# Performance work log

Hardware: AMD Instinct MI355X
Metric: run time of the kernel (lower is better)

## Reference

```python
import math
import jax, jax.numpy as jnp
import numpy as np

N, D, K = 8192, 256, 32


def setup_inputs() -> dict:
    key = jax.random.key(0)
    kx, kw, kb = jax.random.split(key, 3)
    x = jax.random.normal(kx, (N, D), dtype=jnp.float32)
    # params per _init_weights: w ~ N(1, 0.01), b ~ N(0, 0.01)
    w = 1.0 + 0.01 * jax.random.normal(kw, (K, D), dtype=jnp.float32)
    b = 0.01 * jax.random.normal(kb, (K, D), dtype=jnp.float32)
    return {"x": x, "w": w, "b": b}


def reference(x, w, b):
    # x: (N, D); w, b: (K, D)
    y1 = w[None, :, :] * (x[:, None, :] + b[None, :, :])        # (N, K, D)
    y2 = y1 * y1                                                 # (N, K, D)
    y4 = -0.5 * jnp.sum(y2, axis=-1)                             # (N, K)
    gamma = jax.nn.softmax(y4, axis=-1)                          # (N, K)
    y6 = (y2 - 1.0) * (1.0 / math.sqrt(2.0))                     # (N, K, D)
    g = gamma[:, :, None]                                        # (N, K, 1)
    n, kk, d = y1.shape
    sigma_part = (g * y6).reshape(n, kk * d)                     # (N, K*D)
    mu_part = (g * y1).reshape(n, kk * d)                        # (N, K*D)
    phi_patches = jnp.concatenate([sigma_part, mu_part], axis=-1)
    return jnp.mean(phi_patches, axis=0)                         # (2*K*D,)
```

## Files before the change

kernel.cpp:

```cpp
#include <hip/hip_runtime.h>
#include <math.h>

#define Nn 8192
#define Dd 256
#define Kk 32

#define P_OFF   0
#define P2_OFF  4194304
#define SP_OFF  4325376

__global__ __launch_bounds__(1024) void fused_kernel(const float* __restrict__ x,
                                                     const float* __restrict__ w,
                                                     const float* __restrict__ b,
                                                     float* __restrict__ ws) {
    __shared__ __align__(16) float4 uS4[64 * 33];
    __shared__ __align__(16) float4 vS4[64 * 33];
    __shared__ __align__(16) float4 xS4[32 * 64];
    __shared__ float  gS[1024];

    float* P  = ws + P_OFF;
    float* Sp = ws + SP_OFF;
    int tid = threadIdx.x;
    int blk = blockIdx.x;

    {
        const float* xg = x + (size_t)blk * 32 * Dd;
        #pragma unroll
        for (int i = 0; i < 2; ++i) {
            int e4 = tid + i * 1024;
            __builtin_amdgcn_global_load_lds(
                (const __attribute__((address_space(1))) void*)(xg + (size_t)e4 * 4),
                (__attribute__((address_space(3))) void*)(&xS4[e4]),
                16, 0, 0);
        }
    }

    {
        const float4* w4 = (const float4*)w;
        const float4* b4 = (const float4*)b;
        #pragma unroll
        for (int i = 0; i < 2; ++i) {
            int e4 = tid + i * 1024;
            int k  = e4 >> 6;
            int d4 = e4 & 63;
            float4 wv = w4[e4];
            float4 bv = b4[e4];
            float4 vv = {wv.x * bv.x, wv.y * bv.y, wv.z * bv.z, wv.w * bv.w};
            uS4[d4 * 33 + k] = wv;
            vS4[d4 * 33 + k] = vv;
        }
    }
    __syncthreads();

    {
        int lane = tid & 63;
        int wave = tid >> 6;
        int k = lane & 31;
        int h = lane >> 5;
        int r0 = wave * 2;

        const float4* xr0 = &xS4[(r0 + 0) * 64];
        const float4* xr1 = &xS4[(r0 + 1) * 64];

        float4 a0 = {0.f, 0.f, 0.f, 0.f}, a1 = a0;

        #pragma unroll 8
        for (int i = 0; i < 32; ++i) {
            int ii = h * 32 + i;
            float4 u  = uS4[ii * 33 + k];
            float4 v  = vS4[ii * 33 + k];
            float4 x0 = xr0[ii];
            float4 x1 = xr1[ii];
            float y;
            y = fmaf(u.x, x0.x, v.x); a0.x = fmaf(y, y, a0.x);
            y = fmaf(u.y, x0.y, v.y); a0.y = fmaf(y, y, a0.y);
            y = fmaf(u.z, x0.z, v.z); a0.z = fmaf(y, y, a0.z);
            y = fmaf(u.w, x0.w, v.w); a0.w = fmaf(y, y, a0.w);
            y = fmaf(u.x, x1.x, v.x); a1.x = fmaf(y, y, a1.x);
            y = fmaf(u.y, x1.y, v.y); a1.y = fmaf(y, y, a1.y);
            y = fmaf(u.z, x1.z, v.z); a1.z = fmaf(y, y, a1.z);
            y = fmaf(u.w, x1.w, v.w); a1.w = fmaf(y, y, a1.w);
        }

        float s0 = (a0.x + a0.y) + (a0.z + a0.w);
        float s1 = (a1.x + a1.y) + (a1.z + a1.w);
        s0 += __shfl_xor(s0, 32);
        s1 += __shfl_xor(s1, 32);
        float y40 = -0.5f * s0, y41 = -0.5f * s1;

        float m0 = y40, m1 = y41;
        #pragma unroll
        for (int o = 16; o >= 1; o >>= 1) {
            m0 = fmaxf(m0, __shfl_xor(m0, o));
            m1 = fmaxf(m1, __shfl_xor(m1, o));
        }
        float e0 = __expf(y40 - m0), e1 = __expf(y41 - m1);
        float t0 = e0, t1 = e1;
        #pragma unroll
        for (int o = 16; o >= 1; o >>= 1) {
            t0 += __shfl_xor(t0, o);
            t1 += __shfl_xor(t1, o);
        }
        if (h == 0) {
            gS[(r0 + 0) * 32 + k] = e0 / t0;
            gS[(r0 + 1) * 32 + k] = e1 / t1;
        }
    }
    __syncthreads();

    if (tid < 32) {
        float s0 = 0.f, s1 = 0.f, s2 = 0.f, s3 = 0.f;
        #pragma unroll
        for (int r = 0; r < 32; r += 4) {
            s0 += gS[(r + 0) * 32 + tid];
            s1 += gS[(r + 1) * 32 + tid];
            s2 += gS[(r + 2) * 32 + tid];
            s3 += gS[(r + 3) * 32 + tid];
        }
        Sp[tid * 256 + blk] = (s0 + s1) + (s2 + s3);
    }

    {
        int kq = tid >> 8;
        int d  = tid & 255;
        const float* xl = (const float*)xS4;
        const float4* gS4 = (const float4*)gS;

        float aG[8], aH[8];
        #pragma unroll
        for (int j = 0; j < 8; ++j) { aG[j] = 0.f; aH[j] = 0.f; }

        #pragma unroll 4
        for (int r = 0; r < 32; ++r) {
            float xv = xl[r * 256 + d];
            float xx = xv * xv;
            #pragma unroll
            for (int q = 0; q < 2; ++q) {
                float4 gv = gS4[r * 8 + kq * 2 + q];
                aG[4*q+0] = fmaf(gv.x, xv, aG[4*q+0]); aH[4*q+0] = fmaf(gv.x, xx, aH[4*q+0]);
                aG[4*q+1] = fmaf(gv.y, xv, aG[4*q+1]); aH[4*q+1] = fmaf(gv.y, xx, aH[4*q+1]);
                aG[4*q+2] = fmaf(gv.z, xv, aG[4*q+2]); aH[4*q+2] = fmaf(gv.z, xx, aH[4*q+2]);
                aG[4*q+3] = fmaf(gv.w, xv, aG[4*q+3]); aH[4*q+3] = fmaf(gv.w, xx, aH[4*q+3]);
            }
        }

        #pragma unroll
        for (int j = 0; j < 8; ++j) {
            int k = kq * 8 + j;
            P[((size_t)(k * 2 + 0) * 256 + blk) * 256 + d] = aG[j];
            P[((size_t)(k * 2 + 1) * 256 + blk) * 256 + d] = aH[j];
        }
    }
}

__global__ __launch_bounds__(256) void red1_kernel(float* __restrict__ ws) {
    const float* P = ws + P_OFF;
    float* P2 = ws + P2_OFF;
    int tid = threadIdx.x;
    int k  = blockIdx.x >> 4;
    int gh = (blockIdx.x >> 3) & 1;
    int c  = blockIdx.x & 7;

    const float* p = P + ((size_t)(k * 2 + gh) * 256 + c * 32) * 256 + tid;
    float s0 = 0.f, s1 = 0.f, s2 = 0.f, s3 = 0.f;
    #pragma unroll
    for (int i = 0; i < 32; i += 4) {
        s0 += p[(size_t)(i + 0) * 256];
        s1 += p[(size_t)(i + 1) * 256];
        s2 += p[(size_t)(i + 2) * 256];
        s3 += p[(size_t)(i + 3) * 256];
    }
    P2[((size_t)(k * 2 + gh) * 8 + c) * 256 + tid] = (s0 + s1) + (s2 + s3);
}

__global__ __launch_bounds__(256) void red2_kernel(const float* __restrict__ w,
                                                   const float* __restrict__ b,
                                                   const float* __restrict__ ws,
                                                   float* __restrict__ out) {
    const float* P2 = ws + P2_OFF;
    const float* Sp = ws + SP_OFF;
    __shared__ float sred[4];
    int k = blockIdx.x, d = threadIdx.x;

    float sv_part = Sp[k * 256 + d];
    #pragma unroll
    for (int o = 32; o >= 1; o >>= 1) sv_part += __shfl_xor(sv_part, o);
    if ((d & 63) == 0) sred[d >> 6] = sv_part;
    __syncthreads();
    float sv = (sred[0] + sred[1]) + (sred[2] + sred[3]);

    const float* pg = P2 + (size_t)(k * 2 + 0) * 8 * 256 + d;
    const float* ph = P2 + (size_t)(k * 2 + 1) * 8 * 256 + d;
    float Gv = 0.f, Hv = 0.f;
    #pragma unroll
    for (int c = 0; c < 8; ++c) {
        Gv += pg[c * 256];
        Hv += ph[c * 256];
    }

    int idx = k * Dd + d;
    float wv = w[idx], bv = b[idx];
    const float invN = 1.0f / 8192.0f;
    const float c2 = 0.70710678118654752440f * invN;
    float mu = wv * (Gv + bv * sv) * invN;
    float w2 = wv * wv;
    float sg = (w2 * (Hv + 2.0f * bv * Gv + bv * bv * sv) - sv) * c2;
    out[idx] = sg;
    out[Kk * Dd + idx] = mu;
}

extern "C" void kernel_launch(void* const* d_in, const int* in_sizes, int n_in,
                              void* d_out, int out_size, void* d_ws, size_t ws_size,
                              hipStream_t stream) {
    const float* x = (const float*)d_in[0];
    const float* w = (const float*)d_in[1];
    const float* b = (const float*)d_in[2];
    float* out = (float*)d_out;
    float* ws = (float*)d_ws;

    hipLaunchKernelGGL(fused_kernel, dim3(256), dim3(1024), 0, stream, x, w, b, ws);
    hipLaunchKernelGGL(red1_kernel,  dim3(512), dim3(256),  0, stream, ws);
    hipLaunchKernelGGL(red2_kernel,  dim3(32),  dim3(256),  0, stream, w, b, ws, out);
}
```

Before: 82.85 us.

## Reorganize distance phase: 4 rows per thread, XOR-swizzled w/b LDS, async w load

Each thread in the squared-distance phase now computes 4 rows × 1 component over a quarter of D, rather than 2 rows over half of D. This reuses each loaded u/v pair across more rows and cuts LDS traffic per FMA. The w/b tiles move from a padded transposed layout to a row-major layout with an XOR swizzle to avoid bank conflicts, and w is copied straight to LDS with global_load_lds. The change adds an extra LDS buffer and a __syncthreads, because partial sums go through shared memory before the softmax.

```diff
diff --git a/kernel.cpp b/kernel.cpp
--- a/kernel.cpp
+++ b/kernel.cpp
@@ -13,10 +13,11 @@
                                                      const float* __restrict__ w,
                                                      const float* __restrict__ b,
                                                      float* __restrict__ ws) {
-    __shared__ __align__(16) float4 uS4[64 * 33];
-    __shared__ __align__(16) float4 vS4[64 * 33];
-    __shared__ __align__(16) float4 xS4[32 * 64];
-    __shared__ float  gS[1024];
+    __shared__ __align__(16) float4 uS4[2048];
+    __shared__ __align__(16) float4 vS4[2048];
+    __shared__ __align__(16) float4 xS4[2048];
+    __shared__ float hS[1024];
+    __shared__ float gS[1024];
 
     float* P  = ws + P_OFF;
     float* Sp = ws + SP_OFF;
@@ -33,21 +34,31 @@
                 (__attribute__((address_space(3))) void*)(&xS4[e4]),
                 16, 0, 0);
         }
-    }
-
-    {
-        const float4* w4 = (const float4*)w;
-        const float4* b4 = (const float4*)b;
         #pragma unroll
         for (int i = 0; i < 2; ++i) {
             int e4 = tid + i * 1024;
             int k  = e4 >> 6;
-            int d4 = e4 & 63;
-            float4 wv = w4[e4];
-            float4 bv = b4[e4];
-            float4 vv = {wv.x * bv.x, wv.y * bv.y, wv.z * bv.z, wv.w * bv.w};
-            uS4[d4 * 33 + k] = wv;
-            vS4[d4 * 33 + k] = vv;
+            int cc = e4 & 63;
+            int src = cc ^ (k & 7);
+            __builtin_amdgcn_global_load_lds(
+                (const __attribute__((address_space(1))) void*)(w + (size_t)(k * 64 + src) * 4),
+                (__attribute__((address_space(3))) void*)(&uS4[e4]),
+                16, 0, 0);
+        }
+    }
+
+    {
+        const float4* w4 = (const float4*)w;
+        const float4* b4 = (const float4*)b;
+        #pragma unroll
+        for (int i = 0; i < 2; ++i) {
+            int e4 = tid + i * 1024;
+            int k  = e4 >> 6;
+            int cc = e4 & 63;
+            int src = k * 64 + (cc ^ (k & 7));
+            float4 wv = w4[src];
+            float4 bv = b4[src];
+            vS4[e4] = {wv.x * bv.x, wv.y * bv.y, wv.z * bv.z, wv.w * bv.w};
         }
     }
     __syncthreads();
@@ -55,22 +66,29 @@
     {
         int lane = tid & 63;
         int wave = tid >> 6;
-        int k = lane & 31;
-        int h = lane >> 5;
-        int r0 = wave * 2;
-
-        const float4* xr0 = &xS4[(r0 + 0) * 64];
-        const float4* xr1 = &xS4[(r0 + 1) * 64];
-
-        float4 a0 = {0.f, 0.f, 0.f, 0.f}, a1 = a0;
-
-        #pragma unroll 8
-        for (int i = 0; i < 32; ++i) {
-            int ii = h * 32 + i;
-            float4 u  = uS4[ii * 33 + k];
-            float4 v  = vS4[ii * 33 + k];
-            float4 x0 = xr0[ii];
-            float4 x1 = xr1[ii];
+        int kp = lane & 15;
+        int hs = lane >> 4;
+        int kh = wave & 1;
+        int rg = wave >> 1;
+        int k  = kh * 16 + kp;
+        int k7 = k & 7;
+        int r0 = rg * 4;
+
+        const float4* uB = uS4 + k * 64 + hs * 16;
+        const float4* vB = vS4 + k * 64 + hs * 16;
+        const float4* xB = xS4 + r0 * 64 + hs * 16;
+
+        float4 a0 = {0.f, 0.f, 0.f, 0.f}, a1 = a0, a2 = a0, a3 = a0;
+
+        #pragma unroll 4
+        for (int i = 0; i < 16; ++i) {
+            int iu = i ^ k7;
+            float4 u  = uB[iu];
+            float4 v  = vB[iu];
+            float4 x0 = xB[i];
+            float4 x1 = xB[64 + i];
+            float4 x2 = xB[128 + i];
+            float4 x3 = xB[192 + i];
             float y;
             y = fmaf(u.x, x0.x, v.x); a0.x = fmaf(y, y, a0.x);
             y = fmaf(u.y, x0.y, v.y); a0.y = fmaf(y, y, a0.y);
@@ -80,13 +98,43 @@
             y = fmaf(u.y, x1.y, v.y); a1.y = fmaf(y, y, a1.y);
             y = fmaf(u.z, x1.z, v.z); a1.z = fmaf(y, y, a1.z);
             y = fmaf(u.w, x1.w, v.w); a1.w = fmaf(y, y, a1.w);
+            y = fmaf(u.x, x2.x, v.x); a2.x = fmaf(y, y, a2.x);
+            y = fmaf(u.y, x2.y, v.y); a2.y = fmaf(y, y, a2.y);
+            y = fmaf(u.z, x2.z, v.z); a2.z = fmaf(y, y, a2.z);
+            y = fmaf(u.w, x2.w, v.w); a2.w = fmaf(y, y, a2.w);
+            y = fmaf(u.x, x3.x, v.x); a3.x = fmaf(y, y, a3.x);
+            y = fmaf(u.y, x3.y, v.y); a3.y = fmaf(y, y, a3.y);
+            y = fmaf(u.z, x3.z, v.z); a3.z = fmaf(y, y, a3.z);
+            y = fmaf(u.w, x3.w, v.w); a3.w = fmaf(y, y, a3.w);
         }
 
         float s0 = (a0.x + a0.y) + (a0.z + a0.w);
         float s1 = (a1.x + a1.y) + (a1.z + a1.w);
-        s0 += __shfl_xor(s0, 32);
-        s1 += __shfl_xor(s1, 32);
-        float y40 = -0.5f * s0, y41 = -0.5f * s1;
+        float s2 = (a2.x + a2.y) + (a2.z + a2.w);
+        float s3 = (a3.x + a3.y) + (a3.z + a3.w);
+        s0 += __shfl_xor(s0, 16); s0 += __shfl_xor(s0, 32);
+        s1 += __shfl_xor(s1, 16); s1 += __shfl_xor(s1, 32);
+        s2 += __shfl_xor(s2, 16); s2 += __shfl_xor(s2, 32);
+        s3 += __shfl_xor(s3, 16); s3 += __shfl_xor(s3, 32);
+        if (hs == 0) {
+            hS[(r0 + 0) * 32 + k] = s0;
+            hS[(r0 + 1) * 32 + k] = s1;
+            hS[(r0 + 2) * 32 + k] = s2;
+            hS[(r0 + 3) * 32 + k] = s3;
+        }
+    }
+    __syncthreads();
+
+    {
+        int lane = tid & 63;
+        int wave = tid >> 6;
+        int k  = lane & 31;
+        int h2 = lane >> 5;
+        int r0 = wave * 2;
+        int r1 = r0 + 1;
+
+        float y40 = -0.5f * hS[r0 * 32 + k];
+        float y41 = -0.5f * hS[r1 * 32 + k];
 
         float m0 = y40, m1 = y41;
         #pragma unroll
@@ -101,9 +149,9 @@
             t0 += __shfl_xor(t0, o);
             t1 += __shfl_xor(t1, o);
         }
-        if (h == 0) {
-            gS[(r0 + 0) * 32 + k] = e0 / t0;
-            gS[(r0 + 1) * 32 + k] = e1 / t1;
+        if (h2 == 0) {
+            gS[r0 * 32 + k] = e0 / t0;
+            gS[r1 * 32 + k] = e1 / t1;
         }
     }
     __syncthreads();
```

Measured after the change: 83.85 us. No clear change (+1.2%).
